# Optimization experiments

Hardware: AMD Instinct MI355X
Metric: run time of the kernel (lower is better)

## Reference

```python
import jax, jax.numpy as jnp
import numpy as np

B, N, D = 32, 1024, 256

def setup_inputs() -> dict:
    key = jax.random.key(0)
    ks = jax.random.split(key, 7)
    s = 1.0 / np.sqrt(D)
    return {
        "traj": jax.random.normal(ks[0], (B, N, D), dtype=jnp.float32),
        "Wq": jax.random.normal(ks[1], (D, D), dtype=jnp.float32) * s,
        "bq": jax.random.normal(ks[2], (D,), dtype=jnp.float32) * s,
        "Wk": jax.random.normal(ks[3], (D, D), dtype=jnp.float32) * s,
        "bk": jax.random.normal(ks[4], (D,), dtype=jnp.float32) * s,
        "Wv": jax.random.normal(ks[5], (D, D), dtype=jnp.float32) * s,
        "bv": jax.random.normal(ks[6], (D,), dtype=jnp.float32) * s,
    }

def reference(traj, Wq, bq, Wk, bk, Wv, bv):
    # torch nn.Linear: y = x @ W.T + b
    q = jnp.einsum('bnd,ed->bne', traj, Wq) + bq  # [B,N,D]
    k = jnp.einsum('bnd,ed->bne', traj, Wk) + bk  # [B,N,D]
    v = jnp.einsum('bnd,ed->bne', traj, Wv) + bv  # [B,N,D]
    # unscaled dot-product attention (original sums broadcasted Q*K over D)
    scores = jnp.einsum('bnd,bmd->bnm', q, k)     # [B,N,N]
    attn = jax.nn.softmax(scores, axis=-1)        # [B,N,N]
    out = jnp.einsum('bnm,bmd->bnd', attn, v)     # [B,N,D]
    return out
```

## Files before the change

kernel.cpp:

```cpp
#include <hip/hip_runtime.h>

#define NN 1024
#define DD 256

typedef __attribute__((ext_vector_type(8))) _Float16 f16x8;
typedef __attribute__((ext_vector_type(4))) float f32x4;

union H8 { f16x8 v; _Float16 s[8]; };

__device__ __forceinline__ void g2lds16(const void* g, void* l) {
  __builtin_amdgcn_global_load_lds(
      (const __attribute__((address_space(1))) void*)g,
      (__attribute__((address_space(3))) void*)l, 16, 0, 0);
}

__global__ void wconv_kernel(const float* __restrict__ Wq, const float* __restrict__ Wk,
                             const float* __restrict__ Wv, _Float16* __restrict__ pw) {
  int c = blockIdx.x * 256 + threadIdx.x;
  int lane = c & 63;
  int nt = (c >> 6) & 3;
  int kk = (c >> 8) & 7;
  int et = c >> 11;
  int e = et * 64 + nt * 16 + (lane & 15);
  int d = kk * 32 + (lane >> 4) * 8;
  const float* W = (e < 256) ? Wq : (e < 512 ? Wk : Wv);
  const float* src = W + (e & 255) * 256 + d;
  H8 xx;
  for (int j = 0; j < 8; ++j) xx.s[j] = (_Float16)src[j];
  *(f16x8*)(pw + (size_t)c * 8) = xx.v;
}

__global__ __launch_bounds__(256, 2) void proj_kernel(
    const float* __restrict__ traj,
    const float* __restrict__ bq, const float* __restrict__ bk, const float* __restrict__ bv,
    const _Float16* __restrict__ pw,
    _Float16* __restrict__ pq, _Float16* __restrict__ pk, _Float16* __restrict__ pv)
{
  __shared__ _Float16 Wl[2][16384];
  __shared__ _Float16 Cs[64 * 88];

  const int t = threadIdx.x;
  const int lane = t & 63, wave = t >> 6;
  const int col16 = lane & 15, quad = lane >> 4;
  const int mbase = blockIdx.x * 64;
  const int bb = mbase >> 10;

  f16x8 aq[8];
  {
    const float* ap = traj + (size_t)(mbase + wave * 16 + col16) * DD;
    for (int kk = 0; kk < 8; ++kk) {
      float4 u0 = *(const float4*)(ap + kk * 32 + quad * 8);
      float4 u1 = *(const float4*)(ap + kk * 32 + quad * 8 + 4);
      H8 xx;
      xx.s[0] = (_Float16)u0.x; xx.s[1] = (_Float16)u0.y;
      xx.s[2] = (_Float16)u0.z; xx.s[3] = (_Float16)u0.w;
      xx.s[4] = (_Float16)u1.x; xx.s[5] = (_Float16)u1.y;
      xx.s[6] = (_Float16)u1.z; xx.s[7] = (_Float16)u1.w;
      aq[kk] = xx.v;
    }
  }

  const f32x4 zero = {0.f, 0.f, 0.f, 0.f};

  for (int i = 0; i < 8; ++i)
    g2lds16(pw + (size_t)(i * 256 + t) * 8, Wl[0] + (i * 256 + t) * 8);

  for (int et = 0; et < 12; ++et) {
    __syncthreads();
    if (et < 11) {
      const _Float16* ws = pw + (size_t)(et + 1) * 16384;
      _Float16* wd = Wl[(et + 1) & 1];
      for (int i = 0; i < 8; ++i)
        g2lds16(ws + (size_t)(i * 256 + t) * 8, wd + (i * 256 + t) * 8);
    }

    f32x4 acc[4];
    acc[0] = zero; acc[1] = zero; acc[2] = zero; acc[3] = zero;
    {
      const _Float16* wl = Wl[et & 1];
      for (int kk = 0; kk < 8; ++kk)
        for (int nt = 0; nt < 4; ++nt) {
          f16x8 bw = *(const f16x8*)&wl[((kk * 4 + nt) * 64 + lane) * 8];
          acc[nt] = __builtin_amdgcn_mfma_f32_16x16x32_f16(aq[kk], bw, acc[nt], 0, 0, 0);
        }
    }

    int ebase = et * 64;
    int sel = ebase >> 8;
    const float* bias = (sel == 0) ? bq : (sel == 1 ? bk : bv);
    for (int nt = 0; nt < 4; ++nt) {
      float bvl = bias[(ebase & 255) + nt * 16 + col16];
      acc[nt][0] += bvl; acc[nt][1] += bvl; acc[nt][2] += bvl; acc[nt][3] += bvl;
    }

    if (sel < 2) {
      for (int nt = 0; nt < 4; ++nt)
        for (int r = 0; r < 4; ++r)
          Cs[(wave * 16 + quad * 4 + r) * 88 + nt * 16 + col16] = (_Float16)acc[nt][r];
      if (sel == 0) {
        int g = (mbase >> 4) + wave;
        for (int kkloc = 0; kkloc < 2; ++kkloc) {
          f16x8 val = *(const f16x8*)&Cs[(wave * 16 + col16) * 88 + kkloc * 32 + quad * 8];
          *(f16x8*)(pq + (size_t)((g * 8 + et * 2 + kkloc) * 64 + lane) * 8) = val;
        }
      } else {
        int kgg = ((mbase & 1023) >> 4) + wave;
        for (int kk2 = 0; kk2 < 2; ++kk2) {
          f16x8 val = *(const f16x8*)&Cs[(wave * 16 + col16) * 88 + kk2 * 32 + quad * 8];
          int kkg = ((ebase - 256) >> 5) + kk2;
          *(f16x8*)(pk + (size_t)(((bb * 64 + kgg) * 8 + kkg) * 64 + lane) * 8) = val;
        }
      }
    } else {
      for (int nt = 0; nt < 4; ++nt)
        for (int r = 0; r < 4; ++r)
          Cs[(nt * 16 + col16) * 88 + (wave * 16 + quad * 4 + r)] = (_Float16)acc[nt][r];
      __syncthreads();
      int kt64 = (mbase & 1023) >> 6;
      for (int i = 0; i < 2; ++i) {
        int cc = t + i * 256;
        int lane_c = cc & 63, k2 = (cc >> 6) & 1, dtl = cc >> 7;
        f16x8 val = *(const f16x8*)&Cs[(dtl * 16 + (lane_c & 15)) * 88 +
                                       k2 * 32 + (lane_c >> 4) * 8];
        int dtg = ((ebase - 512) >> 4) + dtl;
        int kt32 = kt64 * 2 + k2;
        *(f16x8*)(pv + (size_t)(((bb * 32 + kt32) * 16 + dtg) * 64 + lane_c) * 8) = val;
      }
    }
  }
}

__global__ __launch_bounds__(256, 2) void attn_kernel(
    const _Float16* __restrict__ pq, const _Float16* __restrict__ pk,
    const _Float16* __restrict__ pv, float* __restrict__ out)
{
  __shared__ _Float16 Ks[2][8192];
  __shared__ _Float16 Vs[2][8192];
  __shared__ _Float16 Ps[64 * 40];

  const int t = threadIdx.x;
  const int lane = t & 63, wave = t >> 6;
  const int col16 = lane & 15, quad = lane >> 4;
  const int b = blockIdx.x, qt = blockIdx.y;
  const int qrow0 = b * NN + qt * 64;

  f16x8 aq[8];
  {
    int g = b * 64 + qt * 4 + wave;
    for (int kk = 0; kk < 8; ++kk)
      aq[kk] = *(const f16x8*)(pq + (size_t)((g * 8 + kk) * 64 + lane) * 8);
  }

  float m_i[4], l_i[4], alpha[4];
  f32x4 O[16];
  const f32x4 zero = {0.f, 0.f, 0.f, 0.f};
  for (int r = 0; r < 4; ++r) { m_i[r] = -3.0e38f; l_i[r] = 0.f; }
  for (int dt = 0; dt < 16; ++dt) O[dt] = zero;

  const _Float16* kbb = pk + (size_t)b * 64 * 8 * 64 * 8;
  const _Float16* vbb = pv + (size_t)b * 32 * 16 * 64 * 8;

  for (int i = 0; i < 4; ++i)
    g2lds16(kbb + (size_t)(i * 256 + t) * 8, Ks[0] + (i * 256 + t) * 8);
  for (int i = 0; i < 4; ++i)
    g2lds16(vbb + (size_t)(i * 256 + t) * 8, Vs[0] + (i * 256 + t) * 8);

  for (int kt = 0; kt < 32; ++kt) {
    __syncthreads();
    if (kt < 31) {
      const _Float16* kg = kbb + (size_t)(kt + 1) * 8192;
      const _Float16* vg = vbb + (size_t)(kt + 1) * 8192;
      _Float16* kd = Ks[(kt + 1) & 1];
      _Float16* vd = Vs[(kt + 1) & 1];
      for (int i = 0; i < 4; ++i)
        g2lds16(kg + (size_t)(i * 256 + t) * 8, kd + (i * 256 + t) * 8);
      for (int i = 0; i < 4; ++i)
        g2lds16(vg + (size_t)(i * 256 + t) * 8, vd + (i * 256 + t) * 8);
    }
    const _Float16* ks = Ks[kt & 1];
    const _Float16* vs = Vs[kt & 1];

    f32x4 S[2]; S[0] = zero; S[1] = zero;
    for (int kk = 0; kk < 8; ++kk)
      for (int nt = 0; nt < 2; ++nt) {
        f16x8 bk_ = *(const f16x8*)&ks[((nt * 8 + kk) * 64 + lane) * 8];
        S[nt] = __builtin_amdgcn_mfma_f32_16x16x32_f16(aq[kk], bk_, S[nt], 0, 0, 0);
      }

    for (int r = 0; r < 4; ++r) {
      float vmax = fmaxf(S[0][r], S[1][r]);
      vmax = fmaxf(vmax, __shfl_xor(vmax, 1));
      vmax = fmaxf(vmax, __shfl_xor(vmax, 2));
      vmax = fmaxf(vmax, __shfl_xor(vmax, 4));
      vmax = fmaxf(vmax, __shfl_xor(vmax, 8));
      float nm = fmaxf(m_i[r], vmax);
      alpha[r] = __expf(m_i[r] - nm);
      float p0 = __expf(S[0][r] - nm);
      float p1 = __expf(S[1][r] - nm);
      S[0][r] = p0; S[1][r] = p1;
      float rs = p0 + p1;
      rs += __shfl_xor(rs, 1);
      rs += __shfl_xor(rs, 2);
      rs += __shfl_xor(rs, 4);
      rs += __shfl_xor(rs, 8);
      l_i[r] = l_i[r] * alpha[r] + rs;
      m_i[r] = nm;
    }
    for (int dt = 0; dt < 16; ++dt)
      for (int r = 0; r < 4; ++r) O[dt][r] *= alpha[r];

    for (int nt = 0; nt < 2; ++nt)
      for (int r = 0; r < 4; ++r)
        Ps[(wave * 16 + quad * 4 + r) * 40 + nt * 16 + col16] = (_Float16)S[nt][r];
    f16x8 ap = *(const f16x8*)&Ps[(wave * 16 + col16) * 40 + quad * 8];

    for (int dt = 0; dt < 16; ++dt) {
      f16x8 bv_ = *(const f16x8*)&vs[(dt * 64 + lane) * 8];
      O[dt] = __builtin_amdgcn_mfma_f32_16x16x32_f16(ap, bv_, O[dt], 0, 0, 0);
    }
  }

  for (int r = 0; r < 4; ++r) {
    float inv = 1.0f / l_i[r];
    float* orow = out + (size_t)(qrow0 + wave * 16 + quad * 4 + r) * DD;
    for (int dt = 0; dt < 16; ++dt)
      orow[dt * 16 + col16] = O[dt][r] * inv;
  }
}

extern "C" void kernel_launch(void* const* d_in, const int* in_sizes, int n_in,
                              void* d_out, int out_size, void* d_ws, size_t ws_size,
                              hipStream_t stream) {
  const float* traj = (const float*)d_in[0];
  const float* Wq   = (const float*)d_in[1];
  const float* bq   = (const float*)d_in[2];
  const float* Wk   = (const float*)d_in[3];
  const float* bk   = (const float*)d_in[4];
  const float* Wv   = (const float*)d_in[5];
  const float* bv   = (const float*)d_in[6];

  _Float16* pq = (_Float16*)d_ws;
  _Float16* pk = pq + (size_t)32768 * 256;
  _Float16* pv = pk + (size_t)32768 * 256;
  _Float16* pw = pv + (size_t)32768 * 256;

  wconv_kernel<<<96, 256, 0, stream>>>(Wq, Wk, Wv, pw);
  proj_kernel<<<512, 256, 0, stream>>>(traj, bq, bk, bv, pw, pq, pk, pv);
  attn_kernel<<<dim3(32, 16), 256, 0, stream>>>(pq, pk, pv, (float*)d_out);
}
```

Measured before the change: 182.3 us.

## Retile projection and cut attention LDS and register use for higher occupancy

The projection kernel now gives each block 128 rows and half of the QKV output columns, using 32-column weight tiles. Each wave computes two 16-row tiles that share one weight fragment, and a per-wave staging buffer removes a block barrier. The attention kernel single-buffers V, which is loaded at the start of each iteration, and drops the separate P buffer. This lets the launch bound rise to 3 blocks per SM. Softmax runs in a row-per-lane layout by reusing the consumed K buffer as fp32 scratch, which cuts per-lane state to one max and one sum, and the O rescale is skipped when no row max changed. In exchange there is an extra barrier per iteration, V load latency is less well hidden, and there is more LDS traffic for the transpose.

```diff
diff --git a/kernel.cpp b/kernel.cpp
--- a/kernel.cpp
+++ b/kernel.cpp
@@ -18,10 +18,10 @@
                              const float* __restrict__ Wv, _Float16* __restrict__ pw) {
   int c = blockIdx.x * 256 + threadIdx.x;
   int lane = c & 63;
-  int nt = (c >> 6) & 3;
-  int kk = (c >> 8) & 7;
-  int et = c >> 11;
-  int e = et * 64 + nt * 16 + (lane & 15);
+  int nt = (c >> 6) & 1;
+  int kk = (c >> 7) & 7;
+  int et = c >> 10;
+  int e = et * 32 + nt * 16 + (lane & 15);
   int d = kk * 32 + (lane >> 4) * 8;
   const float* W = (e < 256) ? Wq : (e < 512 ? Wk : Wv);
   const float* src = W + (e & 255) * 256 + d;
@@ -36,18 +36,19 @@
     const _Float16* __restrict__ pw,
     _Float16* __restrict__ pq, _Float16* __restrict__ pk, _Float16* __restrict__ pv)
 {
-  __shared__ _Float16 Wl[2][16384];
-  __shared__ _Float16 Cs[64 * 88];
+  __shared__ alignas(16) _Float16 Wl[2][8192];
+  __shared__ alignas(16) _Float16 Cs[4][1280];
 
   const int t = threadIdx.x;
   const int lane = t & 63, wave = t >> 6;
   const int col16 = lane & 15, quad = lane >> 4;
-  const int mbase = blockIdx.x * 64;
+  const int mt = blockIdx.x >> 1, eh = blockIdx.x & 1;
+  const int mbase = mt * 128;
   const int bb = mbase >> 10;
 
-  f16x8 aq[8];
-  {
-    const float* ap = traj + (size_t)(mbase + wave * 16 + col16) * DD;
+  f16x8 aq[2][8];
+  for (int s = 0; s < 2; ++s) {
+    const float* ap = traj + (size_t)(mbase + wave * 32 + s * 16 + col16) * DD;
     for (int kk = 0; kk < 8; ++kk) {
       float4 u0 = *(const float4*)(ap + kk * 32 + quad * 8);
       float4 u1 = *(const float4*)(ap + kk * 32 + quad * 8 + 4);
@@ -56,87 +57,87 @@
       xx.s[2] = (_Float16)u0.z; xx.s[3] = (_Float16)u0.w;
       xx.s[4] = (_Float16)u1.x; xx.s[5] = (_Float16)u1.y;
       xx.s[6] = (_Float16)u1.z; xx.s[7] = (_Float16)u1.w;
-      aq[kk] = xx.v;
+      aq[s][kk] = xx.v;
     }
   }
 
   const f32x4 zero = {0.f, 0.f, 0.f, 0.f};
-
-  for (int i = 0; i < 8; ++i)
-    g2lds16(pw + (size_t)(i * 256 + t) * 8, Wl[0] + (i * 256 + t) * 8);
-
-  for (int et = 0; et < 12; ++et) {
+  const int et0 = eh * 12;
+
+  for (int i = 0; i < 4; ++i)
+    g2lds16(pw + (size_t)et0 * 8192 + (size_t)(i * 256 + t) * 8, Wl[0] + (i * 256 + t) * 8);
+
+  for (int ei = 0; ei < 12; ++ei) {
     __syncthreads();
-    if (et < 11) {
-      const _Float16* ws = pw + (size_t)(et + 1) * 16384;
-      _Float16* wd = Wl[(et + 1) & 1];
-      for (int i = 0; i < 8; ++i)
+    if (ei < 11) {
+      const _Float16* ws = pw + (size_t)(et0 + ei + 1) * 8192;
+      _Float16* wd = Wl[(ei + 1) & 1];
+      for (int i = 0; i < 4; ++i)
         g2lds16(ws + (size_t)(i * 256 + t) * 8, wd + (i * 256 + t) * 8);
     }
-
-    f32x4 acc[4];
-    acc[0] = zero; acc[1] = zero; acc[2] = zero; acc[3] = zero;
-    {
-      const _Float16* wl = Wl[et & 1];
-      for (int kk = 0; kk < 8; ++kk)
-        for (int nt = 0; nt < 4; ++nt) {
-          f16x8 bw = *(const f16x8*)&wl[((kk * 4 + nt) * 64 + lane) * 8];
-          acc[nt] = __builtin_amdgcn_mfma_f32_16x16x32_f16(aq[kk], bw, acc[nt], 0, 0, 0);
-        }
-    }
-
-    int ebase = et * 64;
-    int sel = ebase >> 8;
+    const _Float16* wl = Wl[ei & 1];
+
+    f32x4 acc[2][2];
+    acc[0][0] = zero; acc[0][1] = zero; acc[1][0] = zero; acc[1][1] = zero;
+    for (int kk = 0; kk < 8; ++kk)
+      for (int nt = 0; nt < 2; ++nt) {
+        f16x8 bw = *(const f16x8*)&wl[((kk * 2 + nt) * 64 + lane) * 8];
+        acc[0][nt] = __builtin_amdgcn_mfma_f32_16x16x32_f16(aq[0][kk], bw, acc[0][nt], 0, 0, 0);
+        acc[1][nt] = __builtin_amdgcn_mfma_f32_16x16x32_f16(aq[1][kk], bw, acc[1][nt], 0, 0, 0);
+      }
+
+    int e0 = eh * 384 + ei * 32;
+    int sel = e0 >> 8;
     const float* bias = (sel == 0) ? bq : (sel == 1 ? bk : bv);
-    for (int nt = 0; nt < 4; ++nt) {
-      float bvl = bias[(ebase & 255) + nt * 16 + col16];
-      acc[nt][0] += bvl; acc[nt][1] += bvl; acc[nt][2] += bvl; acc[nt][3] += bvl;
-    }
-
+    for (int nt = 0; nt < 2; ++nt) {
+      float bvl = bias[(e0 & 255) + nt * 16 + col16];
+      for (int s = 0; s < 2; ++s) {
+        acc[s][nt][0] += bvl; acc[s][nt][1] += bvl;
+        acc[s][nt][2] += bvl; acc[s][nt][3] += bvl;
+      }
+    }
+
+    _Float16* cs = Cs[wave];
     if (sel < 2) {
-      for (int nt = 0; nt < 4; ++nt)
-        for (int r = 0; r < 4; ++r)
-          Cs[(wave * 16 + quad * 4 + r) * 88 + nt * 16 + col16] = (_Float16)acc[nt][r];
+      for (int s = 0; s < 2; ++s)
+        for (int nt = 0; nt < 2; ++nt)
+          for (int r = 0; r < 4; ++r)
+            cs[(s * 16 + quad * 4 + r) * 40 + nt * 16 + col16] = (_Float16)acc[s][nt][r];
       if (sel == 0) {
-        int g = (mbase >> 4) + wave;
-        for (int kkloc = 0; kkloc < 2; ++kkloc) {
-          f16x8 val = *(const f16x8*)&Cs[(wave * 16 + col16) * 88 + kkloc * 32 + quad * 8];
-          *(f16x8*)(pq + (size_t)((g * 8 + et * 2 + kkloc) * 64 + lane) * 8) = val;
+        for (int s = 0; s < 2; ++s) {
+          f16x8 val = *(const f16x8*)&cs[(s * 16 + col16) * 40 + quad * 8];
+          int g = (mbase >> 4) + wave * 2 + s;
+          *(f16x8*)(pq + (size_t)((g * 8 + ei) * 64 + lane) * 8) = val;
         }
       } else {
-        int kgg = ((mbase & 1023) >> 4) + wave;
-        for (int kk2 = 0; kk2 < 2; ++kk2) {
-          f16x8 val = *(const f16x8*)&Cs[(wave * 16 + col16) * 88 + kk2 * 32 + quad * 8];
-          int kkg = ((ebase - 256) >> 5) + kk2;
+        int kkg = (e0 - 256) >> 5;
+        for (int s = 0; s < 2; ++s) {
+          f16x8 val = *(const f16x8*)&cs[(s * 16 + col16) * 40 + quad * 8];
+          int kgg = ((mbase & 1023) >> 4) + wave * 2 + s;
           *(f16x8*)(pk + (size_t)(((bb * 64 + kgg) * 8 + kkg) * 64 + lane) * 8) = val;
         }
       }
     } else {
-      for (int nt = 0; nt < 4; ++nt)
-        for (int r = 0; r < 4; ++r)
-          Cs[(nt * 16 + col16) * 88 + (wave * 16 + quad * 4 + r)] = (_Float16)acc[nt][r];
-      __syncthreads();
-      int kt64 = (mbase & 1023) >> 6;
-      for (int i = 0; i < 2; ++i) {
-        int cc = t + i * 256;
-        int lane_c = cc & 63, k2 = (cc >> 6) & 1, dtl = cc >> 7;
-        f16x8 val = *(const f16x8*)&Cs[(dtl * 16 + (lane_c & 15)) * 88 +
-                                       k2 * 32 + (lane_c >> 4) * 8];
-        int dtg = ((ebase - 512) >> 4) + dtl;
-        int kt32 = kt64 * 2 + k2;
-        *(f16x8*)(pv + (size_t)(((bb * 32 + kt32) * 16 + dtg) * 64 + lane_c) * 8) = val;
-      }
-    }
-  }
-}
-
-__global__ __launch_bounds__(256, 2) void attn_kernel(
+      for (int s = 0; s < 2; ++s)
+        for (int nt = 0; nt < 2; ++nt)
+          for (int r = 0; r < 4; ++r)
+            cs[(nt * 16 + col16) * 40 + s * 16 + quad * 4 + r] = (_Float16)acc[s][nt][r];
+      int kt32 = ((mbase & 1023) >> 5) + wave;
+      for (int dtl = 0; dtl < 2; ++dtl) {
+        f16x8 val = *(const f16x8*)&cs[(dtl * 16 + col16) * 40 + quad * 8];
+        int dtg = ((e0 - 512) >> 4) + dtl;
+        *(f16x8*)(pv + (size_t)(((bb * 32 + kt32) * 16 + dtg) * 64 + lane) * 8) = val;
+      }
+    }
+  }
+}
+
+__global__ __launch_bounds__(256, 3) void attn_kernel(
     const _Float16* __restrict__ pq, const _Float16* __restrict__ pk,
     const _Float16* __restrict__ pv, float* __restrict__ out)
 {
-  __shared__ _Float16 Ks[2][8192];
-  __shared__ _Float16 Vs[2][8192];
-  __shared__ _Float16 Ps[64 * 40];
+  __shared__ alignas(16) _Float16 Ks[2][8192];
+  __shared__ alignas(16) _Float16 Vs[8192];
 
   const int t = threadIdx.x;
   const int lane = t & 63, wave = t >> 6;
@@ -151,10 +152,9 @@
       aq[kk] = *(const f16x8*)(pq + (size_t)((g * 8 + kk) * 64 + lane) * 8);
   }
 
-  float m_i[4], l_i[4], alpha[4];
+  float m_i = -3.0e38f, l_i = 0.f;
   f32x4 O[16];
   const f32x4 zero = {0.f, 0.f, 0.f, 0.f};
-  for (int r = 0; r < 4; ++r) { m_i[r] = -3.0e38f; l_i[r] = 0.f; }
   for (int dt = 0; dt < 16; ++dt) O[dt] = zero;
 
   const _Float16* kbb = pk + (size_t)b * 64 * 8 * 64 * 8;
@@ -162,24 +162,22 @@
 
   for (int i = 0; i < 4; ++i)
     g2lds16(kbb + (size_t)(i * 256 + t) * 8, Ks[0] + (i * 256 + t) * 8);
-  for (int i = 0; i < 4; ++i)
-    g2lds16(vbb + (size_t)(i * 256 + t) * 8, Vs[0] + (i * 256 + t) * 8);
 
   for (int kt = 0; kt < 32; ++kt) {
     __syncthreads();
-    if (kt < 31) {
-      const _Float16* kg = kbb + (size_t)(kt + 1) * 8192;
-      const _Float16* vg = vbb + (size_t)(kt + 1) * 8192;
-      _Float16* kd = Ks[(kt + 1) & 1];
-      _Float16* vd = Vs[(kt + 1) & 1];
+    {
+      const _Float16* vg = vbb + (size_t)kt * 8192;
       for (int i = 0; i < 4; ++i)
-        g2lds16(kg + (size_t)(i * 256 + t) * 8, kd + (i * 256 + t) * 8);
-      for (int i = 0; i < 4; ++i)
-        g2lds16(vg + (size_t)(i * 256 + t) * 8, vd + (i * 256 + t) * 8);
-    }
+        g2lds16(vg + (size_t)(i * 256 + t) * 8, Vs + (i * 256 + t) * 8);
+      if (kt < 31) {
+        const _Float16* kg = kbb + (size_t)(kt + 1) * 8192;
+        _Float16* kd = Ks[(kt + 1) & 1];
+        for (int i = 0; i < 4; ++i)
+          g2lds16(kg + (size_t)(i * 256 + t) * 8, kd + (i * 256 + t) * 8);
+      }
+    }
+
     const _Float16* ks = Ks[kt & 1];
-    const _Float16* vs = Vs[kt & 1];
-
     f32x4 S[2]; S[0] = zero; S[1] = zero;
     for (int kk = 0; kk < 8; ++kk)
       for (int nt = 0; nt < 2; ++nt) {
@@ -187,44 +185,54 @@
         S[nt] = __builtin_amdgcn_mfma_f32_16x16x32_f16(aq[kk], bk_, S[nt], 0, 0, 0);
       }
 
-    for (int r = 0; r < 4; ++r) {
-      float vmax = fmaxf(S[0][r], S[1][r]);
-      vmax = fmaxf(vmax, __shfl_xor(vmax, 1));
-      vmax = fmaxf(vmax, __shfl_xor(vmax, 2));
-      vmax = fmaxf(vmax, __shfl_xor(vmax, 4));
-      vmax = fmaxf(vmax, __shfl_xor(vmax, 8));
-      float nm = fmaxf(m_i[r], vmax);
-      alpha[r] = __expf(m_i[r] - nm);
-      float p0 = __expf(S[0][r] - nm);
-      float p1 = __expf(S[1][r] - nm);
-      S[0][r] = p0; S[1][r] = p1;
-      float rs = p0 + p1;
-      rs += __shfl_xor(rs, 1);
-      rs += __shfl_xor(rs, 2);
-      rs += __shfl_xor(rs, 4);
-      rs += __shfl_xor(rs, 8);
-      l_i[r] = l_i[r] * alpha[r] + rs;
-      m_i[r] = nm;
-    }
-    for (int dt = 0; dt < 16; ++dt)
-      for (int r = 0; r < 4; ++r) O[dt][r] *= alpha[r];
-
+    __syncthreads();
+
+    float* Sp = (float*)Ks[kt & 1];
     for (int nt = 0; nt < 2; ++nt)
       for (int r = 0; r < 4; ++r)
-        Ps[(wave * 16 + quad * 4 + r) * 40 + nt * 16 + col16] = (_Float16)S[nt][r];
-    f16x8 ap = *(const f16x8*)&Ps[(wave * 16 + col16) * 40 + quad * 8];
+        Sp[(wave * 16 + quad * 4 + r) * 36 + nt * 16 + col16] = S[nt][r];
+    float sv[8];
+    *(f32x4*)&sv[0] = *(const f32x4*)&Sp[(wave * 16 + col16) * 36 + quad * 8];
+    *(f32x4*)&sv[4] = *(const f32x4*)&Sp[(wave * 16 + col16) * 36 + quad * 8 + 4];
+
+    float vmax = sv[0];
+    for (int j = 1; j < 8; ++j) vmax = fmaxf(vmax, sv[j]);
+    vmax = fmaxf(vmax, __shfl_xor(vmax, 16));
+    vmax = fmaxf(vmax, __shfl_xor(vmax, 32));
+    float nm = fmaxf(m_i, vmax);
+    float alpha = __expf(m_i - nm);
+    float rs = 0.f;
+    H8 px;
+    for (int j = 0; j < 8; ++j) {
+      float pj = __expf(sv[j] - nm);
+      rs += pj;
+      px.s[j] = (_Float16)pj;
+    }
+    rs += __shfl_xor(rs, 16);
+    rs += __shfl_xor(rs, 32);
+    l_i = l_i * alpha + rs;
+    m_i = nm;
+    f16x8 ap = px.v;
+
+    if (__ballot(alpha < 1.0f)) {
+      float a4[4];
+      for (int r = 0; r < 4; ++r) a4[r] = __shfl(alpha, quad * 4 + r);
+      for (int dt = 0; dt < 16; ++dt)
+        for (int r = 0; r < 4; ++r) O[dt][r] *= a4[r];
+    }
 
     for (int dt = 0; dt < 16; ++dt) {
-      f16x8 bv_ = *(const f16x8*)&vs[(dt * 64 + lane) * 8];
+      f16x8 bv_ = *(const f16x8*)&Vs[(dt * 64 + lane) * 8];
       O[dt] = __builtin_amdgcn_mfma_f32_16x16x32_f16(ap, bv_, O[dt], 0, 0, 0);
     }
   }
 
+  float linv[4];
+  for (int r = 0; r < 4; ++r) linv[r] = 1.0f / __shfl(l_i, quad * 4 + r);
   for (int r = 0; r < 4; ++r) {
-    float inv = 1.0f / l_i[r];
     float* orow = out + (size_t)(qrow0 + wave * 16 + quad * 4 + r) * DD;
     for (int dt = 0; dt < 16; ++dt)
-      orow[dt * 16 + col16] = O[dt][r] * inv;
+      orow[dt * 16 + col16] = O[dt][r] * linv[r];
   }
 }
 
```

Result: faster. 170.3 us (-6.6%).
